# Kernel tuning notes

Measured on AMD Instinct MI355X. Metric: run time of the kernel, lower is better.

Reference implementation:

```python
import jax, jax.numpy as jnp
import numpy as np

N = 50000   # num nodes
E = 800000  # num edges (before self loops)
D = 64      # embed_dim (in == out)
R = 16      # num_relations
EPS = 1e-9


def setup_inputs() -> dict:
    key = jax.random.key(0)
    ks = jax.random.split(key, 8)
    xavier = float(np.sqrt(6.0 / (D + D)))  # xavier_uniform bound for [D, D] fans
    return {
        "x": jax.random.normal(ks[0], (N, D), dtype=jnp.float32),
        "edge_index": jax.random.randint(ks[1], (2, E), 0, N),
        # edge attrs sized E + N to cover self loops added in forward
        "edge_type": jax.random.randint(ks[2], (E + N,), 0, R),
        "path_length": jax.random.uniform(ks[3], (E + N,), jnp.float32, 1.0, 8.0),
        "rel_weight1": jax.random.uniform(ks[4], (R, D, D), jnp.float32, -xavier, xavier),
        "bias1": jnp.zeros((D,), jnp.float32),
        "rel_weight2": jax.random.uniform(ks[5], (R, D, D), jnp.float32, -xavier, xavier),
        "bias2": jnp.zeros((D,), jnp.float32),
        "num_nodes": N,
    }


def _conv(x, src, dst, edge_type, path_length, rel_weight, bias, num_nodes):
    # gather relation-specific weights per edge: [E', D, D]
    w = rel_weight[edge_type]
    # per-edge matvec: x_j @ W_rel -> [E', D]
    msg = jnp.einsum("ei,eio->eo", x[src], w)
    msg = msg / jnp.clip(path_length, EPS, None)[:, None]
    # scatter-add to destination nodes
    aggr = jax.ops.segment_sum(msg, dst, num_segments=num_nodes)
    return jax.nn.relu(aggr + bias)


def reference(x, edge_index, edge_type, path_length, rel_weight1, bias1,
              rel_weight2, bias2, num_nodes):
    loops = jnp.arange(num_nodes)
    src = jnp.concatenate([edge_index[0], loops])  # x_j source (flow src->dst)
    dst = jnp.concatenate([edge_index[1], loops])
    x = _conv(x, src, dst, edge_type, path_length, rel_weight1, bias1, num_nodes)
    x = _conv(x, src, dst, edge_type, path_length, rel_weight2, bias2, num_nodes)
    return x
```

## Files before the change

### kernel.cpp

```cpp
#include <hip/hip_runtime.h>

#define DD 64
#define RR 16
#define EPSF 1e-9f
#define NPB 64
#define BINCH 4096

typedef unsigned short ushort_t;
typedef __bf16 bf16x8 __attribute__((ext_vector_type(8)));
typedef float f32x4 __attribute__((ext_vector_type(4)));
union F8 { uint4 u; bf16x8 v; };

__device__ __forceinline__ void fma4(float4& a, const float4& w, float s) {
    a.x = fmaf(w.x, s, a.x); a.y = fmaf(w.y, s, a.y);
    a.z = fmaf(w.z, s, a.z); a.w = fmaf(w.w, s, a.w);
}

__device__ __forceinline__ unsigned f2bf(float f) {
    unsigned u = __float_as_uint(f);
    return (u + 0x7FFFu + ((u >> 16) & 1u)) >> 16;
}
__device__ __forceinline__ uint2 pk4(float4 v) {
    return make_uint2(f2bf(v.x) | (f2bf(v.y) << 16),
                      f2bf(v.z) | (f2bf(v.w) << 16));
}
__device__ __forceinline__ float bf_lo(unsigned u) { return __uint_as_float(u << 16); }
__device__ __forceinline__ float bf_hi(unsigned u) { return __uint_as_float(u & 0xFFFF0000u); }

__global__ __launch_bounds__(256) void k_packW(
    const float* __restrict__ W, ushort_t* __restrict__ Wb)
{
    int t = blockIdx.x * 256 + threadIdx.x;
    if (t >= RR * 2 * 4 * 64) return;
    int lane = t & 63;
    int ot = (t >> 6) & 3;
    int kb = (t >> 8) & 1;
    int r  = t >> 9;
    int o  = ot * 16 + (lane & 15);
    int k0 = kb * 32 + (lane >> 4) * 8;
    const float* w = W + ((size_t)r * DD + k0) * DD + o;
    unsigned d[4];
    #pragma unroll
    for (int p = 0; p < 4; ++p)
        d[p] = f2bf(w[(2 * p) * DD]) | (f2bf(w[(2 * p + 1) * DD]) << 16);
    ((uint4*)Wb)[t] = make_uint4(d[0], d[1], d[2], d[3]);
}

__global__ __launch_bounds__(256) void k_transform_mfma(
    const float* __restrict__ x, const ushort_t* __restrict__ Wb,
    ushort_t* __restrict__ Y, int N)
{
    const int lane = threadIdx.x & 63;
    const int m0 = (blockIdx.x * 4 + (threadIdx.x >> 6)) * 16;
    if (m0 >= N) return;
    const int quad = lane >> 4, c = lane & 15;

    int node = m0 + c; if (node >= N) node = N - 1;
    const float* xr = x + (size_t)node * DD + quad * 8;
    float4 xa = *(const float4*)xr;
    float4 xb = *(const float4*)(xr + 4);
    float4 xc = *(const float4*)(xr + 32);
    float4 xd = *(const float4*)(xr + 36);
    F8 a0, a1;
    { uint2 p = pk4(xa), q = pk4(xb); a0.u = make_uint4(p.x, p.y, q.x, q.y); }
    { uint2 p = pk4(xc), q = pk4(xd); a1.u = make_uint4(p.x, p.y, q.x, q.y); }

    const uint4* wbp = (const uint4*)Wb + lane;
    const bool full = (m0 + 16 <= N);

    for (int r = 0; r < RR; ++r) {
        ushort_t* yr = Y + ((size_t)r * N + m0) * DD + c;
        #pragma unroll
        for (int ot = 0; ot < 4; ++ot) {
            F8 b0, b1;
            b0.u = wbp[(size_t)(r * 8 + ot) * 64];
            b1.u = wbp[(size_t)(r * 8 + 4 + ot) * 64];
            f32x4 acc = {0.f, 0.f, 0.f, 0.f};
            acc = __builtin_amdgcn_mfma_f32_16x16x32_bf16(a0.v, b0.v, acc, 0, 0, 0);
            acc = __builtin_amdgcn_mfma_f32_16x16x32_bf16(a1.v, b1.v, acc, 0, 0, 0);
            ushort_t* yp = yr + (ot << 4);
            if (full) {
                #pragma unroll
                for (int g = 0; g < 4; ++g)
                    yp[(size_t)(quad * 4 + g) * DD] = (ushort_t)f2bf(acc[g]);
            } else {
                #pragma unroll
                for (int g = 0; g < 4; ++g)
                    if (m0 + quad * 4 + g < N)
                        yp[(size_t)(quad * 4 + g) * DD] = (ushort_t)f2bf(acc[g]);
            }
        }
    }
}


__global__ __launch_bounds__(256) void k_zero_int(int* __restrict__ p, int n)
{
    int i = blockIdx.x * 256 + threadIdx.x;
    if (i < n) p[i] = 0;
}

__global__ __launch_bounds__(256) void k_hist_coarse(
    const int* __restrict__ ei, int* __restrict__ hist, int E, int B)
{
    __shared__ int h[1024];
    for (int i = threadIdx.x; i < B; i += 256) h[i] = 0;
    __syncthreads();
    const int e0 = blockIdx.x * BINCH;
    #pragma unroll 4
    for (int k = 0; k < BINCH / 256; ++k) {
        int e = e0 + k * 256 + threadIdx.x;
        if (e < E) atomicAdd(&h[ei[E + e] >> 6], 1);
    }
    __syncthreads();
    for (int i = threadIdx.x; i < B; i += 256)
        if (h[i]) atomicAdd(&hist[i], h[i]);
}

__global__ __launch_bounds__(256) void k_scan_bucket(
    const int* __restrict__ hist, int* __restrict__ base,
    int* __restrict__ cursor, int B, int E)
{
    __shared__ int sh[256];
    const int t = threadIdx.x;
    int v[4], s = 0;
    #pragma unroll
    for (int k = 0; k < 4; ++k) {
        int i = t * 4 + k;
        v[k] = (i < B) ? hist[i] : 0;
        s += v[k];
    }
    sh[t] = s;
    __syncthreads();
    for (int off = 1; off < 256; off <<= 1) {
        int tmp = (t >= off) ? sh[t - off] : 0;
        __syncthreads();
        sh[t] += tmp;
        __syncthreads();
    }
    int run = sh[t] - s;
    #pragma unroll
    for (int k = 0; k < 4; ++k) {
        int i = t * 4 + k;
        if (i < B) { base[i] = run; cursor[i] = run; }
        run += v[k];
    }
    if (t == 255) base[B] = E;
}

__global__ __launch_bounds__(256) void k_bin(
    const int* __restrict__ ei, const int* __restrict__ et,
    const float* __restrict__ pl, int* __restrict__ cursor,
    uint2* __restrict__ ep, int E, int B)
{
    __shared__ int hl[1024];
    __shared__ int bl[1024];
    for (int i = threadIdx.x; i < B; i += 256) hl[i] = 0;
    __syncthreads();
    const int e0 = blockIdx.x * BINCH;
    #pragma unroll 4
    for (int k = 0; k < BINCH / 256; ++k) {
        int e = e0 + k * 256 + threadIdx.x;
        if (e < E) atomicAdd(&hl[ei[E + e] >> 6], 1);
    }
    __syncthreads();
    for (int i = threadIdx.x; i < B; i += 256) {
        int c = hl[i];
        bl[i] = c ? atomicAdd(&cursor[i], c) : 0;
        hl[i] = 0;
    }
    __syncthreads();
    #pragma unroll 2
    for (int k = 0; k < BINCH / 256; ++k) {
        int e = e0 + k * 256 + threadIdx.x;
        if (e < E) {
            int dst = ei[E + e];
            int b = dst >> 6;
            int rank = atomicAdd(&hl[b], 1);
            int src = ei[e];
            int rt  = et[e];
            float iv = 1.0f / fmaxf(pl[e], EPSF);
            ep[bl[b] + rank] = make_uint2(
                (unsigned)src | ((unsigned)rt << 16) | ((unsigned)(dst & 63) << 20),
                __float_as_uint(iv));
        }
    }
}

__global__ __launch_bounds__(256) void k_sortb(
    const uint2* __restrict__ ep, const int* __restrict__ base,
    uint2* __restrict__ ep2, int* __restrict__ rowptr, int N, int B)
{
    __shared__ int hist[NPB];
    __shared__ int off[NPB];
    const int b = blockIdx.x, tid = threadIdx.x;
    const int beg = base[b], end = base[b + 1];
    if (tid < NPB) hist[tid] = 0;
    __syncthreads();
    for (int p = beg + tid; p < end; p += 256)
        atomicAdd(&hist[(ep[p].x >> 20) & 63u], 1);
    __syncthreads();
    if (tid == 0) {
        int run = 0;
        #pragma unroll
        for (int i = 0; i < NPB; ++i) { off[i] = run; run += hist[i]; }
    }
    __syncthreads();
    if (tid < NPB) {
        int n = b * NPB + tid;
        if (n <= N) rowptr[n] = beg + off[tid];
        hist[tid] = 0;
    }
    __syncthreads();
    for (int p = beg + tid; p < end; p += 256) {
        uint2 m = ep[p];
        int d = (m.x >> 20) & 63u;
        int rank = atomicAdd(&hist[d], 1);
        ep2[beg + off[d] + rank] = make_uint2(m.x & 0xFFFFFu, m.y);
    }
}

__global__ __launch_bounds__(256) void k_aggregate(
    const ushort_t* __restrict__ Y, const int* __restrict__ rowptr,
    const uint2* __restrict__ ep,
    const int* __restrict__ et, const float* __restrict__ pl,
    const float* __restrict__ bias, float* __restrict__ out, int N, int E)
{
    const int n = blockIdx.x * 8 + (threadIdx.x >> 5);
    const int lane = threadIdx.x & 31;
    if (n >= N) return;

    int rts = et[E + n];
    float ivs = 1.0f / fmaxf(pl[E + n], EPSF);
    unsigned yv = *(const unsigned*)(Y + ((size_t)rts * N + n) * DD + 2 * lane);
    float accx = bf_lo(yv) * ivs;
    float accy = bf_hi(yv) * ivs;

    const int beg = rowptr[n], end = rowptr[n + 1];
    for (int p0 = beg; p0 < end; p0 += 32) {
        int cnt = end - p0; if (cnt > 32) cnt = 32;
        unsigned pk = 0, ivb = 0;
        if (lane < cnt) { uint2 m = ep[p0 + lane]; pk = m.x; ivb = m.y; }
        int jj = 0;
        for (; jj + 4 <= cnt; jj += 4) {
            unsigned v[4]; float ivv[4];
            #pragma unroll
            for (int q = 0; q < 4; ++q) {
                unsigned pkj = (unsigned)__shfl((int)pk, jj + q, 32);
                ivv[q] = __uint_as_float((unsigned)__shfl((int)ivb, jj + q, 32));
                v[q] = *(const unsigned*)(Y +
                    (((size_t)((pkj >> 16) & 15u)) * N + (pkj & 0xFFFFu)) * DD + 2 * lane);
            }
            #pragma unroll
            for (int q = 0; q < 4; ++q) {
                accx = fmaf(bf_lo(v[q]), ivv[q], accx);
                accy = fmaf(bf_hi(v[q]), ivv[q], accy);
            }
        }
        for (; jj < cnt; ++jj) {
            unsigned pkj = (unsigned)__shfl((int)pk, jj, 32);
            float ivj = __uint_as_float((unsigned)__shfl((int)ivb, jj, 32));
            unsigned v = *(const unsigned*)(Y +
                (((size_t)((pkj >> 16) & 15u)) * N + (pkj & 0xFFFFu)) * DD + 2 * lane);
            accx = fmaf(bf_lo(v), ivj, accx);
            accy = fmaf(bf_hi(v), ivj, accy);
        }
    }
    float2 bb = *(const float2*)(bias + 2 * lane);
    float2 o;
    o.x = fmaxf(accx + bb.x, 0.f);
    o.y = fmaxf(accy + bb.y, 0.f);
    *(float2*)(out + (size_t)n * DD + 2 * lane) = o;
}


__global__ __launch_bounds__(256) void k_transform(
    const float* __restrict__ x, const float* __restrict__ W,
    ushort_t* __restrict__ Y, int N, int r_base, int r_cnt, int yr_off)
{
    __shared__ float xt[DD * 128];
    __shared__ float ws[DD * DD];
    const int n0 = blockIdx.x * 128;
    const int tid = threadIdx.x;

    #pragma unroll
    for (int c = 0; c < 8; ++c) {
        int idx = c * 256 + tid;
        int n  = idx >> 4;
        int i4 = (idx & 15) << 2;
        int gn = n0 + n;
        float4 v = make_float4(0.f, 0.f, 0.f, 0.f);
        if (gn < N) v = ((const float4*)(x + (size_t)gn * DD))[idx & 15];
        int n4 = n >> 2, nr = n & 3;
        float vv[4] = {v.x, v.y, v.z, v.w};
        #pragma unroll
        for (int k = 0; k < 4; ++k) {
            int i = i4 + k;
            int swz = (i >> 2) & 7;
            xt[i * 128 + (((n4 ^ swz) << 2) | nr)] = vv[k];
        }
    }

    const int j  = tid & 15;
    const int nq = tid >> 4;

    for (int rr = 0; rr < r_cnt; ++rr) {
        const int r = r_base + blockIdx.y * r_cnt + rr;
        __syncthreads();
        {
            const float4* Wv = (const float4*)(W + (size_t)r * DD * DD);
            float4* wv = (float4*)ws;
            #pragma unroll
            for (int c = 0; c < 4; ++c) wv[c * 256 + tid] = Wv[c * 256 + tid];
        }
        __syncthreads();

        float4 acc[8];
        #pragma unroll
        for (int m = 0; m < 8; ++m) acc[m] = make_float4(0.f, 0.f, 0.f, 0.f);

        #pragma unroll 4
        for (int i = 0; i < DD; ++i) {
            const int swz = (i >> 2) & 7;
            const float4 wv = *(const float4*)&ws[i * DD + 4 * j];
            #pragma unroll
            for (int h = 0; h < 2; ++h) {
                const int col4 = (2 * nq + h) ^ swz;
                const float4 xv = *(const float4*)&xt[i * 128 + (col4 << 2)];
                fma4(acc[4 * h + 0], wv, xv.x);
                fma4(acc[4 * h + 1], wv, xv.y);
                fma4(acc[4 * h + 2], wv, xv.z);
                fma4(acc[4 * h + 3], wv, xv.w);
            }
        }

        const size_t ybase = (size_t)(r - yr_off) * N;
        #pragma unroll
        for (int m = 0; m < 8; ++m) {
            int node = n0 + 8 * nq + 4 * (m >> 2) + (m & 3);
            if (node < N)
                *(uint2*)(Y + (ybase + node) * DD + 4 * j) = pk4(acc[m]);
        }
    }
}

__global__ __launch_bounds__(256) void k_edges(
    const int* __restrict__ ei, const int* __restrict__ et,
    const float* __restrict__ pl, const ushort_t* __restrict__ Y,
    float* __restrict__ aggr, int N, int E, int Etot, int rel_filter)
{
    int sub = threadIdx.x >> 5;
    int lane = threadIdx.x & 31;
    int e = blockIdx.x * 8 + sub;
    if (e >= Etot) return;
    int rt = et[e];
    int yrel = rt;
    if (rel_filter >= 0) { if (rt != rel_filter) return; yrel = 0; }
    int src, dst;
    if (e < E) { src = ei[e]; dst = ei[E + e]; }
    else       { src = dst = e - E; }
    float inv = 1.0f / fmaxf(pl[e], EPSF);
    unsigned v = *(const unsigned*)(Y + ((size_t)yrel * N + src) * DD + 2 * lane);
    atomicAdd(&aggr[(size_t)dst * DD + 2 * lane],     bf_lo(v) * inv);
    atomicAdd(&aggr[(size_t)dst * DD + 2 * lane + 1], bf_hi(v) * inv);
}

__global__ __launch_bounds__(256) void k_bias_relu(
    const float* __restrict__ aggr, const float* __restrict__ bias,
    float* __restrict__ out, int N)
{
    int idx = blockIdx.x * 256 + threadIdx.x;
    if (idx >= N * (DD / 4)) return;
    float4 a = ((const float4*)aggr)[idx];
    int o4 = (idx & 15) * 4;
    a.x = fmaxf(a.x + bias[o4 + 0], 0.f);
    a.y = fmaxf(a.y + bias[o4 + 1], 0.f);
    a.z = fmaxf(a.z + bias[o4 + 2], 0.f);
    a.w = fmaxf(a.w + bias[o4 + 3], 0.f);
    ((float4*)out)[idx] = a;
}

__global__ __launch_bounds__(256) void k_zero(float* __restrict__ p, size_t n)
{
    size_t i = (size_t)blockIdx.x * 256 + threadIdx.x;
    size_t stride = (size_t)gridDim.x * 256;
    for (; i < n; i += stride) p[i] = 0.f;
}

extern "C" void kernel_launch(void* const* d_in, const int* in_sizes, int n_in,
                              void* d_out, int out_size, void* d_ws, size_t ws_size,
                              hipStream_t stream)
{
    const float* x  = (const float*)d_in[0];
    const int*   ei = (const int*)d_in[1];
    const int*   et = (const int*)d_in[2];
    const float* pl = (const float*)d_in[3];
    const float* W1 = (const float*)d_in[4];
    const float* b1 = (const float*)d_in[5];
    const float* W2 = (const float*)d_in[6];
    const float* b2 = (const float*)d_in[7];
    float* out = (float*)d_out;

    const int N = in_sizes[0] / DD;
    const int E = in_sizes[1] / 2;
    const size_t ndf = (size_t)N * DD;
    const size_t wb_elems = (size_t)RR * 2 * 4 * 64 * 8;
    const int B = (N + NPB - 1) / NPB;

    char* wsb = (char*)d_ws;
    ushort_t* Y   = (ushort_t*)wsb;
    float* aggr1  = (float*)(wsb + (size_t)RR * ndf * 2);
    ushort_t* Wb1 = (ushort_t*)((char*)aggr1 + ndf * 4);
    ushort_t* Wb2 = Wb1 + wb_elems;
    uint2* ep     = (uint2*)(Wb2 + wb_elems);
    uint2* ep2    = ep + E;
    int* hist     = (int*)(ep2 + E);
    int* base     = hist + B;
    int* cursor   = base + (B + 1);
    int* rowptr   = cursor + B;

    const size_t need_main = (size_t)RR * ndf * 2 + ndf * 4 + wb_elems * 4 +
        (size_t)E * 16 + ((size_t)B * 3 + 1 + (size_t)N + 1) * 4;
    const bool main_ok = (ws_size >= need_main) && (N <= 65535) && (B <= 1024);

    if (main_ok) {
        const int gBin = (E + BINCH - 1) / BINCH;
        k_packW<<<(RR * 2 * 4 * 64 + 255) / 256, 256, 0, stream>>>(W1, Wb1);
        k_packW<<<(RR * 2 * 4 * 64 + 255) / 256, 256, 0, stream>>>(W2, Wb2);
        k_zero_int<<<(B + 255) / 256, 256, 0, stream>>>(hist, B);
        k_hist_coarse<<<gBin, 256, 0, stream>>>(ei, hist, E, B);
        k_scan_bucket<<<1, 256, 0, stream>>>(hist, base, cursor, B, E);
        k_bin<<<gBin, 256, 0, stream>>>(ei, et, pl, cursor, ep, E, B);
        k_sortb<<<B, 256, 0, stream>>>(ep, base, ep2, rowptr, N, B);

        const int gT = (N + 63) / 64;
        const int gA = (N + 7) / 8;
        for (int layer = 0; layer < 2; ++layer) {
            const float* xin   = layer ? aggr1 : x;
            const ushort_t* Wb = layer ? Wb2 : Wb1;
            const float* bias  = layer ? b2 : b1;
            float* dest        = layer ? out : aggr1;
            k_transform_mfma<<<gT, 256, 0, stream>>>(xin, Wb, Y, N);
            k_aggregate<<<gA, 256, 0, stream>>>(Y, rowptr, ep2, et, pl,
                                                bias, dest, N, E);
        }
        return;
    }

    ushort_t* Yc = (ushort_t*)wsb;
    float* ag    = (float*)(wsb + ndf * 2);
    const int gx     = (N + 127) / 128;
    const int gEdgeT = (E + N + 7) / 8;
    const int gQuad  = (N * (DD / 4) + 255) / 256;
    float* hid = ag;

    for (int layer = 0; layer < 2; ++layer) {
        const float* xin  = layer ? hid : x;
        const float* W    = layer ? W2 : W1;
        const float* bias = layer ? b2 : b1;
        float* aggr       = layer ? out : ag;
        k_zero<<<1024, 256, 0, stream>>>(aggr, ndf);
        for (int r = 0; r < RR; ++r) {
            k_transform<<<dim3(gx, 1), 256, 0, stream>>>(xin, W, Yc, N, r, 1, r);
            k_edges<<<gEdgeT, 256, 0, stream>>>(ei, et, pl, Yc, aggr, N, E, E + N, r);
        }
        k_bias_relu<<<gQuad, 256, 0, stream>>>(aggr, bias, layer ? out : hid, N);
    }
}
```

Before: 252.2 us.

## Aggregate per-relation inputs in LDS then apply one fused MFMA transform

```diff
diff --git a/kernel.cpp b/kernel.cpp
--- a/kernel.cpp
+++ b/kernel.cpp
@@ -3,7 +3,6 @@
 #define DD 64
 #define RR 16
 #define EPSF 1e-9f
-#define NPB 64
 #define BINCH 4096
 
 typedef unsigned short ushort_t;
@@ -15,7 +14,6 @@
     a.x = fmaf(w.x, s, a.x); a.y = fmaf(w.y, s, a.y);
     a.z = fmaf(w.z, s, a.z); a.w = fmaf(w.w, s, a.w);
 }
-
 __device__ __forceinline__ unsigned f2bf(float f) {
     unsigned u = __float_as_uint(f);
     return (u + 0x7FFFu + ((u >> 16) & 1u)) >> 16;
@@ -26,6 +24,15 @@
 }
 __device__ __forceinline__ float bf_lo(unsigned u) { return __uint_as_float(u << 16); }
 __device__ __forceinline__ float bf_hi(unsigned u) { return __uint_as_float(u & 0xFFFF0000u); }
+
+__global__ __launch_bounds__(256) void k_cast(
+    const float* __restrict__ x, ushort_t* __restrict__ xb, int n4)
+{
+    int i = blockIdx.x * 256 + threadIdx.x;
+    if (i >= n4) return;
+    float4 v = ((const float4*)x)[i];
+    ((uint2*)xb)[i] = pk4(v);
+}
 
 __global__ __launch_bounds__(256) void k_packW(
     const float* __restrict__ W, ushort_t* __restrict__ Wb)
@@ -43,56 +50,8 @@
     #pragma unroll
     for (int p = 0; p < 4; ++p)
         d[p] = f2bf(w[(2 * p) * DD]) | (f2bf(w[(2 * p + 1) * DD]) << 16);
-    ((uint4*)Wb)[t] = make_uint4(d[0], d[1], d[2], d[3]);
-}
-
-__global__ __launch_bounds__(256) void k_transform_mfma(
-    const float* __restrict__ x, const ushort_t* __restrict__ Wb,
-    ushort_t* __restrict__ Y, int N)
-{
-    const int lane = threadIdx.x & 63;
-    const int m0 = (blockIdx.x * 4 + (threadIdx.x >> 6)) * 16;
-    if (m0 >= N) return;
-    const int quad = lane >> 4, c = lane & 15;
-
-    int node = m0 + c; if (node >= N) node = N - 1;
-    const float* xr = x + (size_t)node * DD + quad * 8;
-    float4 xa = *(const float4*)xr;
-    float4 xb = *(const float4*)(xr + 4);
-    float4 xc = *(const float4*)(xr + 32);
-    float4 xd = *(const float4*)(xr + 36);
-    F8 a0, a1;
-    { uint2 p = pk4(xa), q = pk4(xb); a0.u = make_uint4(p.x, p.y, q.x, q.y); }
-    { uint2 p = pk4(xc), q = pk4(xd); a1.u = make_uint4(p.x, p.y, q.x, q.y); }
-
-    const uint4* wbp = (const uint4*)Wb + lane;
-    const bool full = (m0 + 16 <= N);
-
-    for (int r = 0; r < RR; ++r) {
-        ushort_t* yr = Y + ((size_t)r * N + m0) * DD + c;
-        #pragma unroll
-        for (int ot = 0; ot < 4; ++ot) {
-            F8 b0, b1;
-            b0.u = wbp[(size_t)(r * 8 + ot) * 64];
-            b1.u = wbp[(size_t)(r * 8 + 4 + ot) * 64];
-            f32x4 acc = {0.f, 0.f, 0.f, 0.f};
-            acc = __builtin_amdgcn_mfma_f32_16x16x32_bf16(a0.v, b0.v, acc, 0, 0, 0);
-            acc = __builtin_amdgcn_mfma_f32_16x16x32_bf16(a1.v, b1.v, acc, 0, 0, 0);
-            ushort_t* yp = yr + (ot << 4);
-            if (full) {
-                #pragma unroll
-                for (int g = 0; g < 4; ++g)
-                    yp[(size_t)(quad * 4 + g) * DD] = (ushort_t)f2bf(acc[g]);
-            } else {
-                #pragma unroll
-                for (int g = 0; g < 4; ++g)
-                    if (m0 + quad * 4 + g < N)
-                        yp[(size_t)(quad * 4 + g) * DD] = (ushort_t)f2bf(acc[g]);
-            }
-        }
-    }
-}
-
+    ((uint4*)Wb)[(((r * 2 + kb) * 4 + ot) * 64) + lane] = make_uint4(d[0], d[1], d[2], d[3]);
+}
 
 __global__ __launch_bounds__(256) void k_zero_int(int* __restrict__ p, int n)
 {
@@ -187,92 +146,134 @@
     }
 }
 
-__global__ __launch_bounds__(256) void k_sortb(
+__global__ __launch_bounds__(256) void k_split(
     const uint2* __restrict__ ep, const int* __restrict__ base,
-    uint2* __restrict__ ep2, int* __restrict__ rowptr, int N, int B)
-{
-    __shared__ int hist[NPB];
-    __shared__ int off[NPB];
+    uint2* __restrict__ ep2, int* __restrict__ base2, int B)
+{
+    __shared__ int h4[4], off[4], cur[4];
     const int b = blockIdx.x, tid = threadIdx.x;
     const int beg = base[b], end = base[b + 1];
-    if (tid < NPB) hist[tid] = 0;
+    if (tid < 4) h4[tid] = 0;
     __syncthreads();
     for (int p = beg + tid; p < end; p += 256)
-        atomicAdd(&hist[(ep[p].x >> 20) & 63u], 1);
+        atomicAdd(&h4[(ep[p].x >> 24) & 3u], 1);
     __syncthreads();
     if (tid == 0) {
         int run = 0;
         #pragma unroll
-        for (int i = 0; i < NPB; ++i) { off[i] = run; run += hist[i]; }
-    }
-    __syncthreads();
-    if (tid < NPB) {
-        int n = b * NPB + tid;
-        if (n <= N) rowptr[n] = beg + off[tid];
-        hist[tid] = 0;
-    }
-    __syncthreads();
+        for (int s = 0; s < 4; ++s) { off[s] = run; cur[s] = 0; run += h4[s]; }
+    }
+    __syncthreads();
+    if (tid < 4) base2[b * 4 + tid] = beg + off[tid];
     for (int p = beg + tid; p < end; p += 256) {
         uint2 m = ep[p];
-        int d = (m.x >> 20) & 63u;
-        int rank = atomicAdd(&hist[d], 1);
-        ep2[beg + off[d] + rank] = make_uint2(m.x & 0xFFFFFu, m.y);
-    }
-}
-
-__global__ __launch_bounds__(256) void k_aggregate(
-    const ushort_t* __restrict__ Y, const int* __restrict__ rowptr,
-    const uint2* __restrict__ ep,
+        int s = (m.x >> 24) & 3u;
+        int rank = atomicAdd(&cur[s], 1);
+        ep2[beg + off[s] + rank] = make_uint2(m.x & 0x00FFFFFFu, m.y);
+    }
+}
+
+__global__ __launch_bounds__(256) void k_fused(
+    const ushort_t* __restrict__ xb, const ushort_t* __restrict__ Wb,
+    const int* __restrict__ base2, const uint2* __restrict__ ep2,
     const int* __restrict__ et, const float* __restrict__ pl,
-    const float* __restrict__ bias, float* __restrict__ out, int N, int E)
-{
-    const int n = blockIdx.x * 8 + (threadIdx.x >> 5);
-    const int lane = threadIdx.x & 31;
-    if (n >= N) return;
-
-    int rts = et[E + n];
-    float ivs = 1.0f / fmaxf(pl[E + n], EPSF);
-    unsigned yv = *(const unsigned*)(Y + ((size_t)rts * N + n) * DD + 2 * lane);
-    float accx = bf_lo(yv) * ivs;
-    float accy = bf_hi(yv) * ivs;
-
-    const int beg = rowptr[n], end = rowptr[n + 1];
-    for (int p0 = beg; p0 < end; p0 += 32) {
+    const float* __restrict__ bias, float* __restrict__ out32,
+    ushort_t* __restrict__ out16, int N, int E, int write32)
+{
+    __shared__ float S[16 * 1024];
+    const int tid = threadIdx.x;
+    const int n0 = blockIdx.x * 16;
+
+    #pragma unroll
+    for (int i = tid; i < 16 * 1024; i += 256) S[i] = 0.f;
+    __syncthreads();
+
+    const int hw = tid >> 5;
+    const int lane = tid & 31;
+
+    #pragma unroll
+    for (int t = 0; t < 2; ++t) {
+        int n = n0 + 2 * hw + t;
+        if (n < N) {
+            int rt = et[E + n];
+            float iv = 1.0f / fmaxf(pl[E + n], EPSF);
+            unsigned v = *(const unsigned*)(xb + (size_t)n * DD + 2 * lane);
+            int loc = 2 * hw + t;
+            int chunk = rt * 16 + (lane >> 1);
+            int addr = loc * 1024 + ((chunk ^ (loc & 7)) << 2) + ((2 * lane) & 3);
+            atomicAdd(&S[addr],     bf_lo(v) * iv);
+            atomicAdd(&S[addr + 1], bf_hi(v) * iv);
+        }
+    }
+
+    const int beg = base2[blockIdx.x], end = base2[blockIdx.x + 1];
+    for (int p0 = beg + hw * 32; p0 < end; p0 += 256) {
         int cnt = end - p0; if (cnt > 32) cnt = 32;
         unsigned pk = 0, ivb = 0;
-        if (lane < cnt) { uint2 m = ep[p0 + lane]; pk = m.x; ivb = m.y; }
+        if (lane < cnt) { uint2 m = ep2[p0 + lane]; pk = m.x; ivb = m.y; }
         int jj = 0;
-        for (; jj + 4 <= cnt; jj += 4) {
-            unsigned v[4]; float ivv[4];
+        for (; jj + 8 <= cnt; jj += 8) {
+            unsigned v[8], pkk[8]; float ivv[8];
             #pragma unroll
-            for (int q = 0; q < 4; ++q) {
-                unsigned pkj = (unsigned)__shfl((int)pk, jj + q, 32);
+            for (int q = 0; q < 8; ++q) {
+                pkk[q] = (unsigned)__shfl((int)pk, jj + q, 32);
                 ivv[q] = __uint_as_float((unsigned)__shfl((int)ivb, jj + q, 32));
-                v[q] = *(const unsigned*)(Y +
-                    (((size_t)((pkj >> 16) & 15u)) * N + (pkj & 0xFFFFu)) * DD + 2 * lane);
+                v[q] = *(const unsigned*)(xb + (size_t)(pkk[q] & 0xFFFFu) * DD + 2 * lane);
             }
             #pragma unroll
-            for (int q = 0; q < 4; ++q) {
-                accx = fmaf(bf_lo(v[q]), ivv[q], accx);
-                accy = fmaf(bf_hi(v[q]), ivv[q], accy);
+            for (int q = 0; q < 8; ++q) {
+                int rt  = (pkk[q] >> 16) & 15u;
+                int loc = (pkk[q] >> 20) & 15u;
+                int chunk = rt * 16 + (lane >> 1);
+                int addr = loc * 1024 + ((chunk ^ (loc & 7)) << 2) + ((2 * lane) & 3);
+                atomicAdd(&S[addr],     bf_lo(v[q]) * ivv[q]);
+                atomicAdd(&S[addr + 1], bf_hi(v[q]) * ivv[q]);
             }
         }
         for (; jj < cnt; ++jj) {
             unsigned pkj = (unsigned)__shfl((int)pk, jj, 32);
             float ivj = __uint_as_float((unsigned)__shfl((int)ivb, jj, 32));
-            unsigned v = *(const unsigned*)(Y +
-                (((size_t)((pkj >> 16) & 15u)) * N + (pkj & 0xFFFFu)) * DD + 2 * lane);
-            accx = fmaf(bf_lo(v), ivj, accx);
-            accy = fmaf(bf_hi(v), ivj, accy);
-        }
-    }
-    float2 bb = *(const float2*)(bias + 2 * lane);
-    float2 o;
-    o.x = fmaxf(accx + bb.x, 0.f);
-    o.y = fmaxf(accy + bb.y, 0.f);
-    *(float2*)(out + (size_t)n * DD + 2 * lane) = o;
-}
-
+            unsigned v = *(const unsigned*)(xb + (size_t)(pkj & 0xFFFFu) * DD + 2 * lane);
+            int rt  = (pkj >> 16) & 15u;
+            int loc = (pkj >> 20) & 15u;
+            int chunk = rt * 16 + (lane >> 1);
+            int addr = loc * 1024 + ((chunk ^ (loc & 7)) << 2) + ((2 * lane) & 3);
+            atomicAdd(&S[addr],     bf_lo(v) * ivj);
+            atomicAdd(&S[addr + 1], bf_hi(v) * ivj);
+        }
+    }
+    __syncthreads();
+
+    const int wv = tid >> 6;
+    const int l64 = tid & 63;
+    const int m = l64 & 15, quad = l64 >> 4;
+    const int sig = m & 7;
+
+    f32x4 acc = {0.f, 0.f, 0.f, 0.f};
+    const uint4* wbp = (const uint4*)Wb;
+    #pragma unroll 4
+    for (int kb = 0; kb < 32; ++kb) {
+        int c0 = kb * 8 + quad * 2;
+        float4 alo = *(const float4*)&S[m * 1024 + ((c0 ^ sig) << 2)];
+        float4 ahi = *(const float4*)&S[m * 1024 + (((c0 + 1) ^ sig) << 2)];
+        F8 a;
+        { uint2 p = pk4(alo), q = pk4(ahi); a.u = make_uint4(p.x, p.y, q.x, q.y); }
+        F8 b; b.u = wbp[(size_t)(kb * 4 + wv) * 64 + l64];
+        acc = __builtin_amdgcn_mfma_f32_16x16x32_bf16(a.v, b.v, acc, 0, 0, 0);
+    }
+
+    const int o = wv * 16 + m;
+    const float bo = bias[o];
+    #pragma unroll
+    for (int g = 0; g < 4; ++g) {
+        int n = n0 + quad * 4 + g;
+        if (n < N) {
+            float val = fmaxf(acc[g] + bo, 0.f);
+            if (write32) out32[(size_t)n * DD + o] = val;
+            else         out16[(size_t)n * DD + o] = (ushort_t)f2bf(val);
+        }
+    }
+}
 
 __global__ __launch_bounds__(256) void k_transform(
     const float* __restrict__ x, const float* __restrict__ W,
@@ -405,45 +406,40 @@
     const int E = in_sizes[1] / 2;
     const size_t ndf = (size_t)N * DD;
     const size_t wb_elems = (size_t)RR * 2 * 4 * 64 * 8;
-    const int B = (N + NPB - 1) / NPB;
+    const int B  = (N + 63) / 64;
+    const int B2 = (N + 15) / 16;
 
     char* wsb = (char*)d_ws;
-    ushort_t* Y   = (ushort_t*)wsb;
-    float* aggr1  = (float*)(wsb + (size_t)RR * ndf * 2);
-    ushort_t* Wb1 = (ushort_t*)((char*)aggr1 + ndf * 4);
+    ushort_t* xb  = (ushort_t*)wsb;
+    ushort_t* hb  = xb + ndf;
+    ushort_t* Wb1 = hb + ndf;
     ushort_t* Wb2 = Wb1 + wb_elems;
     uint2* ep     = (uint2*)(Wb2 + wb_elems);
     uint2* ep2    = ep + E;
     int* hist     = (int*)(ep2 + E);
     int* base     = hist + B;
     int* cursor   = base + (B + 1);
-    int* rowptr   = cursor + B;
-
-    const size_t need_main = (size_t)RR * ndf * 2 + ndf * 4 + wb_elems * 4 +
-        (size_t)E * 16 + ((size_t)B * 3 + 1 + (size_t)N + 1) * 4;
+    int* base2    = cursor + B;
+
+    const size_t need_main = ndf * 4 + wb_elems * 4 + (size_t)E * 16 +
+        ((size_t)B * 3 + 1 + (size_t)B * 4 + 2) * 4;
     const bool main_ok = (ws_size >= need_main) && (N <= 65535) && (B <= 1024);
 
     if (main_ok) {
         const int gBin = (E + BINCH - 1) / BINCH;
+        k_cast<<<((int)(ndf / 4) + 255) / 256, 256, 0, stream>>>(x, xb, (int)(ndf / 4));
         k_packW<<<(RR * 2 * 4 * 64 + 255) / 256, 256, 0, stream>>>(W1, Wb1);
         k_packW<<<(RR * 2 * 4 * 64 + 255) / 256, 256, 0, stream>>>(W2, Wb2);
         k_zero_int<<<(B + 255) / 256, 256, 0, stream>>>(hist, B);
         k_hist_coarse<<<gBin, 256, 0, stream>>>(ei, hist, E, B);
         k_scan_bucket<<<1, 256, 0, stream>>>(hist, base, cursor, B, E);
         k_bin<<<gBin, 256, 0, stream>>>(ei, et, pl, cursor, ep, E, B);
-        k_sortb<<<B, 256, 0, stream>>>(ep, base, ep2, rowptr, N, B);
-
-        const int gT = (N + 63) / 64;
-        const int gA = (N + 7) / 8;
-        for (int layer = 0; layer < 2; ++layer) {
-            const float* xin   = layer ? aggr1 : x;
-            const ushort_t* Wb = layer ? Wb2 : Wb1;
-            const float* bias  = layer ? b2 : b1;
-            float* dest        = layer ? out : aggr1;
-            k_transform_mfma<<<gT, 256, 0, stream>>>(xin, Wb, Y, N);
-            k_aggregate<<<gA, 256, 0, stream>>>(Y, rowptr, ep2, et, pl,
-                                                bias, dest, N, E);
-        }
+        k_split<<<B, 256, 0, stream>>>(ep, base, ep2, base2, B);
+
+        k_fused<<<B2, 256, 0, stream>>>(xb, Wb1, base2, ep2, et, pl, b1,
+                                        nullptr, hb, N, E, 0);
+        k_fused<<<B2, 256, 0, stream>>>(hb, Wb2, base2, ep2, et, pl, b2,
+                                        out, nullptr, N, E, 1);
         return;
     }
 
```

Measured after the change: 804.1 us. 219% more time.
